# Performance work log

Hardware: AMD Instinct MI355X
Metric: run time of the kernel (lower is better)

## Reference

```python
import jax, jax.numpy as jnp
import numpy as np

N = 100000
E = 600000
D_IN, D_HID, D_OUT = 128, 128, 64


def setup_inputs() -> dict:
    key = jax.random.key(0)
    k1, k2, k3, k4 = jax.random.split(key, 4)
    x = jax.random.normal(k1, (N, D_IN), dtype=jnp.float32)
    edge_index = jax.random.randint(k2, (2, E), 0, N, dtype=jnp.int64)
    edge_weight = jnp.ones((E,), dtype=jnp.float32)
    W1 = jax.random.normal(k3, (D_IN, D_HID), dtype=jnp.float32) / np.sqrt(D_IN)
    b1 = jnp.zeros((D_HID,), dtype=jnp.float32)
    W2 = jax.random.normal(k4, (D_HID, D_OUT), dtype=jnp.float32) / np.sqrt(D_HID)
    b2 = jnp.zeros((D_OUT,), dtype=jnp.float32)
    return {"x": x, "edge_index": edge_index, "edge_weight": edge_weight,
            "W1": W1, "b1": b1, "W2": W2, "b2": b2}


def _gcn_conv(x, row, col, ew, W, b, n_nodes):
    # x: [N, d_in]; row/col/ew include self loops. PyG gcn_norm:
    # deg[i] = sum of ew over edges with target i; norm = d^-1/2[row]*ew*d^-1/2[col]
    deg = jax.ops.segment_sum(ew, col, num_segments=n_nodes)
    dinv = jnp.where(deg > 0, jax.lax.rsqrt(deg), 0.0)
    norm = dinv[row] * ew * dinv[col]  # [E+N]
    xw = x @ W  # dense transform first (d_out <= d_in path)
    msg = xw[row] * norm[:, None]  # gather + scale  [E+N, d_out]
    out = jax.ops.segment_sum(msg, col, num_segments=n_nodes)  # scatter-add
    return out + b


def reference(x, edge_index, edge_weight, W1, b1, W2, b2):
    n = x.shape[0]
    loops = jnp.arange(n, dtype=edge_index.dtype)
    row = jnp.concatenate([edge_index[0], loops])
    col = jnp.concatenate([edge_index[1], loops])
    ew = jnp.concatenate([edge_weight, jnp.ones((n,), dtype=edge_weight.dtype)])
    # dropout is identity in eval mode
    h = jax.nn.relu(_gcn_conv(x, row, col, ew, W1, b1, n))
    out = _gcn_conv(h, row, col, ew, W2, b2, n)
    return out
```

## Files before the change

### kernel.cpp

```cpp
#include <hip/hip_runtime.h>


constexpr int SCAN_BLOCKS = 256;

typedef __attribute__((ext_vector_type(8))) short short8;
typedef __attribute__((ext_vector_type(4))) float f32x4;

__device__ __forceinline__ ushort f2bf(float f) {
    unsigned u = __float_as_uint(f);
    return (ushort)((u + 0x7fffu + ((u >> 16) & 1u)) >> 16);
}
__device__ __forceinline__ float bf2f(ushort h) {
    return __uint_as_float((unsigned)h << 16);
}

__global__ __launch_bounds__(256) void prep_kernel(
        int* __restrict__ cnt, int N,
        const float* __restrict__ W2, ushort* __restrict__ W2t) {
    const int n4 = (N >> 2) + 1;
    const int nbz = (n4 + 255) / 256;
    int b = blockIdx.x;
    if (b < nbz) {
        const int i = b * 256 + threadIdx.x;
        if (i < n4) reinterpret_cast<int4*>(cnt)[i] = make_int4(0, 0, 0, 0);
        return;
    }
    b -= nbz;
    const int o = b * 256 + threadIdx.x;
    if (o < 64 * 128)
        W2t[o] = f2bf(W2[(size_t)(o & 127) * 64 + (o >> 7)]);
}

__global__ __launch_bounds__(256, 2) void combo_kernel(
        const float* __restrict__ X, const float* __restrict__ W1,
        ushort* __restrict__ Ab, int N, int G,
        const int* __restrict__ col, int* __restrict__ cnt,
        int* __restrict__ rank, int E) {
    __shared__ __align__(16) ushort sX[128 * 128];
    __shared__ __align__(16) ushort sW[128 * 128];
    const int tid = threadIdx.x;

    if (blockIdx.x >= G) {
        const int e4 = ((blockIdx.x - G) * 256 + tid) * 4;
        if (e4 + 3 < E) {
            const int4 c4 = *reinterpret_cast<const int4*>(col + e4);
            int4 r4;
            r4.x = atomicAdd(&cnt[c4.x], 1);
            r4.y = atomicAdd(&cnt[c4.y], 1);
            r4.z = atomicAdd(&cnt[c4.z], 1);
            r4.w = atomicAdd(&cnt[c4.w], 1);
            *reinterpret_cast<int4*>(rank + e4) = r4;
        } else {
            for (int e = e4; e < E; e++) rank[e] = atomicAdd(&cnt[col[e]], 1);
        }
        return;
    }

    const int base = blockIdx.x * 128;
    #pragma unroll
    for (int p = 0; p < 8; p++) {
        const int ch = p * 256 + tid;
        const int r = ch >> 4, cpos = ch & 15;
        const int grow = base + r;
        uint4 u = make_uint4(0, 0, 0, 0);
        if (grow < N) {
            const float* xp = X + (size_t)grow * 128 + cpos * 8;
            const float4 a = *reinterpret_cast<const float4*>(xp);
            const float4 c = *reinterpret_cast<const float4*>(xp + 4);
            u.x = (uint)f2bf(a.x) | ((uint)f2bf(a.y) << 16);
            u.y = (uint)f2bf(a.z) | ((uint)f2bf(a.w) << 16);
            u.z = (uint)f2bf(c.x) | ((uint)f2bf(c.y) << 16);
            u.w = (uint)f2bf(c.z) | ((uint)f2bf(c.w) << 16);
        }
        const int b = (cpos * 16) ^ ((r & 7) << 4);
        *reinterpret_cast<uint4*>(reinterpret_cast<char*>(sX) + r * 256 + b) = u;
    }
    #pragma unroll
    for (int p = 0; p < 8; p++) {
        const int ch = p * 256 + tid;
        const int c = ch & 127, kc = ch >> 7;
        const int k0 = kc * 8;
        float f[8];
        #pragma unroll
        for (int j = 0; j < 8; j++) f[j] = W1[(size_t)(k0 + j) * 128 + c];
        uint4 u;
        u.x = (uint)f2bf(f[0]) | ((uint)f2bf(f[1]) << 16);
        u.y = (uint)f2bf(f[2]) | ((uint)f2bf(f[3]) << 16);
        u.z = (uint)f2bf(f[4]) | ((uint)f2bf(f[5]) << 16);
        u.w = (uint)f2bf(f[6]) | ((uint)f2bf(f[7]) << 16);
        const int b = (k0 * 2) ^ ((c & 7) << 4);
        *reinterpret_cast<uint4*>(reinterpret_cast<char*>(sW) + c * 256 + b) = u;
    }
    __syncthreads();

    const int lane = tid & 63;
    const int wid = tid >> 6;
    const int wr = wid >> 1;
    const int wc = wid & 1;
    const int lr = lane & 15;
    const int g  = lane >> 4;

    f32x4 acc[4][4];
    #pragma unroll
    for (int i = 0; i < 4; i++)
        #pragma unroll
        for (int f = 0; f < 4; f++) acc[i][f] = (f32x4){0.f, 0.f, 0.f, 0.f};

    #pragma unroll
    for (int ks = 0; ks < 4; ks++) {
        const int koff = ks * 64 + g * 16;
        short8 a[4], b[4];
        #pragma unroll
        for (int i = 0; i < 4; i++) {
            const int r = wr * 64 + i * 16 + lr;
            a[i] = *reinterpret_cast<const short8*>(
                reinterpret_cast<const char*>(sX) + r * 256 + (koff ^ ((r & 7) << 4)));
        }
        #pragma unroll
        for (int f = 0; f < 4; f++) {
            const int c = wc * 64 + f * 16 + lr;
            b[f] = *reinterpret_cast<const short8*>(
                reinterpret_cast<const char*>(sW) + c * 256 + (koff ^ ((c & 7) << 4)));
        }
        #pragma unroll
        for (int i = 0; i < 4; i++)
            #pragma unroll
            for (int f = 0; f < 4; f++)
                acc[i][f] = __builtin_amdgcn_mfma_f32_16x16x32_bf16(a[i], b[f], acc[i][f], 0, 0, 0);
    }

    #pragma unroll
    for (int i = 0; i < 4; i++)
        #pragma unroll
        for (int reg = 0; reg < 4; reg++) {
            const int grow = base + wr * 64 + i * 16 + g * 4 + reg;
            if (grow < N)
                #pragma unroll
                for (int f = 0; f < 4; f++)
                    Ab[(size_t)grow * 128 + wc * 64 + f * 16 + lr] = f2bf(acc[i][f][reg]);
        }
}

__global__ __launch_bounds__(256) void scan_kernel(
        const int* __restrict__ cnt, int* __restrict__ rowptr,
        int* __restrict__ partial, int* __restrict__ flag, int N, int E) {
    const int t = threadIdx.x, b = blockIdx.x;
    const int T = SCAN_BLOCKS * 256;
    const int chunk = (N + T - 1) / T;
    const int j = b * 256 + t;
    const int s = min(j * chunk, N), e = min(s + chunk, N);
    int acc = 0;
    for (int i = s; i < e; i++) acc += cnt[i];

    __shared__ int sh[256];
    sh[t] = acc;
    __syncthreads();
    for (int off = 1; off < 256; off <<= 1) {
        int x = sh[t];
        int a = (t >= off) ? sh[t - off] : 0;
        __syncthreads();
        sh[t] = x + a;
        __syncthreads();
    }
    const int thr_excl = sh[t] - acc;
    if (t == 255) partial[b] = sh[255];
    __syncthreads();
    if (t == 0) {
        __threadfence();
        atomicAdd(flag, 1);
        while (__hip_atomic_load(flag, __ATOMIC_RELAXED,
                                 __HIP_MEMORY_SCOPE_AGENT) < SCAN_BLOCKS) {}
    }
    __syncthreads();

    __shared__ int tp[256];
    tp[t] = __hip_atomic_load(&partial[t], __ATOMIC_RELAXED,
                              __HIP_MEMORY_SCOPE_AGENT);
    __syncthreads();
    for (int off = 1; off < 256; off <<= 1) {
        int x = tp[t];
        int a = (t >= off) ? tp[t - off] : 0;
        __syncthreads();
        tp[t] = x + a;
        __syncthreads();
    }
    int run = ((b == 0) ? 0 : tp[b - 1]) + thr_excl;
    for (int i = s; i < e; i++) { rowptr[i] = run; run += cnt[i]; }
    if (j == 0) rowptr[N] = E;
}

__global__ void fill_kernel(const int* __restrict__ row, const int* __restrict__ col,
        const float* __restrict__ ew, const int* __restrict__ rowptr,
        const int* __restrict__ rank, int2* __restrict__ csr, int E) {
    const int e4 = (blockIdx.x * blockDim.x + threadIdx.x) * 4;
    if (e4 + 3 < E) {
        const int4 c4 = *reinterpret_cast<const int4*>(col + e4);
        const int4 r4 = *reinterpret_cast<const int4*>(row + e4);
        const int4 w4 = *reinterpret_cast<const int4*>((const int*)ew + e4);
        const int4 k4 = *reinterpret_cast<const int4*>(rank + e4);
        const int p0 = rowptr[c4.x] + k4.x;
        const int p1 = rowptr[c4.y] + k4.y;
        const int p2 = rowptr[c4.z] + k4.z;
        const int p3 = rowptr[c4.w] + k4.w;
        csr[p0] = make_int2(r4.x, w4.x);
        csr[p1] = make_int2(r4.y, w4.y);
        csr[p2] = make_int2(r4.z, w4.z);
        csr[p3] = make_int2(r4.w, w4.w);
    } else {
        for (int e = e4; e < E; e++)
            csr[rowptr[col[e]] + rank[e]] = make_int2(row[e], __float_as_int(ew[e]));
    }
}

__global__ __launch_bounds__(256) void degsum_kernel(
        const int* __restrict__ rowptr, const int2* __restrict__ csr,
        float* __restrict__ dinv, int N) {
    const int n = blockIdx.x * blockDim.x + threadIdx.x;
    if (n >= N) return;
    const int e0 = rowptr[n], e1 = rowptr[n + 1];
    float d = 1.0f;
    for (int e = e0; e < e1; e++) d += __int_as_float(csr[e].y);
    dinv[n] = (d > 0.0f) ? rsqrtf(d) : 0.0f;
}

__global__ __launch_bounds__(256) void agg1_kernel(
        const int* __restrict__ rowptr, const int2* __restrict__ csr,
        const float* __restrict__ dinv,
        const ushort* __restrict__ src, const float* __restrict__ bias,
        ushort* __restrict__ dst, int N) {
    const int gid = blockIdx.x * 256 + threadIdx.x;
    const int c = gid >> 4;
    if (c >= N) return;
    const int lane = gid & 15;
    const float di = dinv[c];
    const float sl = di * di;
    float acc[8];
    {
        const short8 s8 = *reinterpret_cast<const short8*>(src + (size_t)c * 128 + lane * 8);
        #pragma unroll
        for (int j = 0; j < 8; j++) acc[j] = bf2f((ushort)s8[j]) * sl;
    }
    const int e0 = rowptr[c], e1 = rowptr[c + 1];
    int e = e0;
    for (; e + 4 <= e1; e += 4) {
        const int2 c0 = csr[e], c1 = csr[e + 1], c2 = csr[e + 2], c3 = csr[e + 3];
        const float w0 = __int_as_float(c0.y) * dinv[c0.x] * di;
        const float w1 = __int_as_float(c1.y) * dinv[c1.x] * di;
        const float w2 = __int_as_float(c2.y) * dinv[c2.x] * di;
        const float w3 = __int_as_float(c3.y) * dinv[c3.x] * di;
        const short8 v0 = *reinterpret_cast<const short8*>(src + (size_t)c0.x * 128 + lane * 8);
        const short8 v1 = *reinterpret_cast<const short8*>(src + (size_t)c1.x * 128 + lane * 8);
        const short8 v2 = *reinterpret_cast<const short8*>(src + (size_t)c2.x * 128 + lane * 8);
        const short8 v3 = *reinterpret_cast<const short8*>(src + (size_t)c3.x * 128 + lane * 8);
        #pragma unroll
        for (int j = 0; j < 8; j++)
            acc[j] += bf2f((ushort)v0[j]) * w0 + bf2f((ushort)v1[j]) * w1 +
                      bf2f((ushort)v2[j]) * w2 + bf2f((ushort)v3[j]) * w3;
    }
    for (; e < e1; e++) {
        const int2 ce = csr[e];
        const float w = __int_as_float(ce.y) * dinv[ce.x] * di;
        const short8 v = *reinterpret_cast<const short8*>(src + (size_t)ce.x * 128 + lane * 8);
        #pragma unroll
        for (int j = 0; j < 8; j++) acc[j] += bf2f((ushort)v[j]) * w;
    }
    const float4 b0 = reinterpret_cast<const float4*>(bias)[lane * 2];
    const float4 b1 = reinterpret_cast<const float4*>(bias)[lane * 2 + 1];
    acc[0] = fmaxf(acc[0] + b0.x, 0.f); acc[1] = fmaxf(acc[1] + b0.y, 0.f);
    acc[2] = fmaxf(acc[2] + b0.z, 0.f); acc[3] = fmaxf(acc[3] + b0.w, 0.f);
    acc[4] = fmaxf(acc[4] + b1.x, 0.f); acc[5] = fmaxf(acc[5] + b1.y, 0.f);
    acc[6] = fmaxf(acc[6] + b1.z, 0.f); acc[7] = fmaxf(acc[7] + b1.w, 0.f);
    uint4 o;
    o.x = (uint)f2bf(acc[0]) | ((uint)f2bf(acc[1]) << 16);
    o.y = (uint)f2bf(acc[2]) | ((uint)f2bf(acc[3]) << 16);
    o.z = (uint)f2bf(acc[4]) | ((uint)f2bf(acc[5]) << 16);
    o.w = (uint)f2bf(acc[6]) | ((uint)f2bf(acc[7]) << 16);
    *reinterpret_cast<uint4*>(dst + (size_t)c * 128 + lane * 8) = o;
}

__global__ __launch_bounds__(256, 2) void gemm2_kernel(
        const ushort* __restrict__ Xb, const ushort* __restrict__ Wt,
        ushort* __restrict__ Y, int N) {
    __shared__ __align__(16) ushort sX[128 * 128];
    __shared__ __align__(16) ushort sW[64 * 128];
    const int tid = threadIdx.x;
    const int base = blockIdx.x * 128;

    #pragma unroll
    for (int p = 0; p < 8; p++) {
        const int ch = p * 256 + tid;
        const int r = ch >> 4, cpos = ch & 15;
        const int grow = base + r;
        uint4 v = make_uint4(0, 0, 0, 0);
        if (grow < N)
            v = *reinterpret_cast<const uint4*>(Xb + (size_t)grow * 128 + cpos * 8);
        const int b = (cpos * 16) ^ ((r & 7) << 4);
        *reinterpret_cast<uint4*>(reinterpret_cast<char*>(sX) + r * 256 + b) = v;
    }
    #pragma unroll
    for (int p = 0; p < 4; p++) {
        const int ch = p * 256 + tid;
        const int r = ch >> 4, cpos = ch & 15;
        uint4 v = *reinterpret_cast<const uint4*>(Wt + (size_t)r * 128 + cpos * 8);
        const int b = (cpos * 16) ^ ((r & 7) << 4);
        *reinterpret_cast<uint4*>(reinterpret_cast<char*>(sW) + r * 256 + b) = v;
    }
    __syncthreads();

    const int lane = tid & 63;
    const int wid = tid >> 6;
    const int lr = lane & 15;
    const int g  = lane >> 4;

    f32x4 acc[2][4];
    #pragma unroll
    for (int i = 0; i < 2; i++)
        #pragma unroll
        for (int f = 0; f < 4; f++) acc[i][f] = (f32x4){0.f, 0.f, 0.f, 0.f};

    #pragma unroll
    for (int ks = 0; ks < 4; ks++) {
        const int koff = ks * 64 + g * 16;
        short8 a[2], b[4];
        #pragma unroll
        for (int i = 0; i < 2; i++) {
            const int r = wid * 32 + i * 16 + lr;
            a[i] = *reinterpret_cast<const short8*>(
                reinterpret_cast<const char*>(sX) + r * 256 + (koff ^ ((r & 7) << 4)));
        }
        #pragma unroll
        for (int f = 0; f < 4; f++) {
            const int c = f * 16 + lr;
            b[f] = *reinterpret_cast<const short8*>(
                reinterpret_cast<const char*>(sW) + c * 256 + (koff ^ ((c & 7) << 4)));
        }
        #pragma unroll
        for (int i = 0; i < 2; i++)
            #pragma unroll
            for (int f = 0; f < 4; f++)
                acc[i][f] = __builtin_amdgcn_mfma_f32_16x16x32_bf16(a[i], b[f], acc[i][f], 0, 0, 0);
    }

    #pragma unroll
    for (int i = 0; i < 2; i++)
        #pragma unroll
        for (int reg = 0; reg < 4; reg++) {
            const int grow = base + wid * 32 + i * 16 + g * 4 + reg;
            if (grow < N)
                #pragma unroll
                for (int f = 0; f < 4; f++)
                    Y[(size_t)grow * 64 + f * 16 + lr] = f2bf(acc[i][f][reg]);
        }
}

__global__ __launch_bounds__(256) void agg2_kernel(
        const int* __restrict__ rowptr, const int2* __restrict__ csr,
        const float* __restrict__ dinv,
        const ushort* __restrict__ src, const float* __restrict__ bias,
        float* __restrict__ dst, int N) {
    const int gid = blockIdx.x * 256 + threadIdx.x;
    const int c = gid >> 3;
    if (c >= N) return;
    const int lane = gid & 7;
    const float di = dinv[c];
    const float sl = di * di;
    float acc[8];
    {
        const short8 s8 = *reinterpret_cast<const short8*>(src + (size_t)c * 64 + lane * 8);
        #pragma unroll
        for (int j = 0; j < 8; j++) acc[j] = bf2f((ushort)s8[j]) * sl;
    }
    const int e0 = rowptr[c], e1 = rowptr[c + 1];
    int e = e0;
    for (; e + 4 <= e1; e += 4) {
        const int2 c0 = csr[e], c1 = csr[e + 1], c2 = csr[e + 2], c3 = csr[e + 3];
        const float w0 = __int_as_float(c0.y) * dinv[c0.x] * di;
        const float w1 = __int_as_float(c1.y) * dinv[c1.x] * di;
        const float w2 = __int_as_float(c2.y) * dinv[c2.x] * di;
        const float w3 = __int_as_float(c3.y) * dinv[c3.x] * di;
        const short8 v0 = *reinterpret_cast<const short8*>(src + (size_t)c0.x * 64 + lane * 8);
        const short8 v1 = *reinterpret_cast<const short8*>(src + (size_t)c1.x * 64 + lane * 8);
        const short8 v2 = *reinterpret_cast<const short8*>(src + (size_t)c2.x * 64 + lane * 8);
        const short8 v3 = *reinterpret_cast<const short8*>(src + (size_t)c3.x * 64 + lane * 8);
        #pragma unroll
        for (int j = 0; j < 8; j++)
            acc[j] += bf2f((ushort)v0[j]) * w0 + bf2f((ushort)v1[j]) * w1 +
                      bf2f((ushort)v2[j]) * w2 + bf2f((ushort)v3[j]) * w3;
    }
    for (; e < e1; e++) {
        const int2 ce = csr[e];
        const float w = __int_as_float(ce.y) * dinv[ce.x] * di;
        const short8 v = *reinterpret_cast<const short8*>(src + (size_t)ce.x * 64 + lane * 8);
        #pragma unroll
        for (int j = 0; j < 8; j++) acc[j] += bf2f((ushort)v[j]) * w;
    }
    const float4 b0 = reinterpret_cast<const float4*>(bias)[lane * 2];
    const float4 b1 = reinterpret_cast<const float4*>(bias)[lane * 2 + 1];
    float* dp = dst + (size_t)c * 64 + lane * 8;
    *reinterpret_cast<float4*>(dp) =
        make_float4(acc[0] + b0.x, acc[1] + b0.y, acc[2] + b0.z, acc[3] + b0.w);
    *reinterpret_cast<float4*>(dp + 4) =
        make_float4(acc[4] + b1.x, acc[5] + b1.y, acc[6] + b1.z, acc[7] + b1.w);
}

extern "C" void kernel_launch(void* const* d_in, const int* in_sizes, int n_in,
                              void* d_out, int out_size, void* d_ws, size_t ws_size,
                              hipStream_t stream) {
    const float* x  = (const float*)d_in[0];
    const int*   ei = (const int*)d_in[1];
    const float* ew = (const float*)d_in[2];
    const float* W1 = (const float*)d_in[3];
    const float* b1 = (const float*)d_in[4];
    const float* W2 = (const float*)d_in[5];
    const float* b2 = (const float*)d_in[6];
    const int N = in_sizes[0] / 128;
    const int E = in_sizes[1] / 2;
    const int* row = ei;
    const int* col = ei + E;

    char* w = (char*)d_ws;
    float* dinv = (float*)w;                 w += (size_t)N * 4;
    ushort* Ab  = (ushort*)w;                w += (size_t)N * 256;
    ushort* Hb  = (ushort*)w;                w += (size_t)N * 256;
    ushort* Gb  = (ushort*)w;                w += (size_t)N * 128;
    ushort* W2t = (ushort*)w;                w += 64 * 128 * 2;
    int* cnt    = (int*)w;                   w += (size_t)N * 4 + 16;
    int* rowptr = (int*)w;                   w += (size_t)(N + 8) * 4;
    int* partial= (int*)w;                   w += 2048 * 4;
    int* rank   = (int*)w;                   w += (size_t)E * 4;
    int2* csr   = (int2*)w;
    float* out  = (float*)d_out;
    int* flag   = cnt + N;

    const int ntiles = (N + 127) / 128;
    const int nbz = ((N >> 2) + 1 + 255) / 256;
    const int eb4 = (E / 4 + 255) / 256;

    prep_kernel<<<nbz + 32, 256, 0, stream>>>(cnt, N, W2, W2t);
    combo_kernel<<<ntiles + eb4, 256, 0, stream>>>(x, W1, Ab, N, ntiles,
                                                   col, cnt, rank, E);
    scan_kernel<<<SCAN_BLOCKS, 256, 0, stream>>>(cnt, rowptr, partial, flag, N, E);
    fill_kernel<<<eb4, 256, 0, stream>>>(row, col, ew, rowptr, rank, csr, E);
    degsum_kernel<<<(N + 255) / 256, 256, 0, stream>>>(rowptr, csr, dinv, N);
    agg1_kernel<<<(N * 16 + 255) / 256, 256, 0, stream>>>(rowptr, csr, dinv, Ab, b1, Hb, N);
    gemm2_kernel<<<ntiles, 256, 0, stream>>>(Hb, W2t, Gb, N);
    agg2_kernel<<<(N * 8 + 255) / 256, 256, 0, stream>>>(rowptr, csr, dinv, Gb, b2, out, N);
}
```

Before: 142.7 us.

## Fuse scan, CSR fill and degree into one kernel with grid barriers

Moves the cnt zeroing and W2 transpose into the GEMM1 launch and splits edge counting into its own kernel. Scan, CSR fill and degree computation now run in a single persistent 256-block kernel separated by software grid barriers. The aim is to cut launch overhead and inter-kernel gaps. In exchange, fill and degree work runs on only 256 blocks with grid-stride loops, which may lower parallelism, and the counting atomics no longer overlap with the GEMM.

```diff
diff --git a/kernel.cpp b/kernel.cpp
--- a/kernel.cpp
+++ b/kernel.cpp
@@ -14,44 +14,38 @@
     return __uint_as_float((unsigned)h << 16);
 }
 
-__global__ __launch_bounds__(256) void prep_kernel(
-        int* __restrict__ cnt, int N,
-        const float* __restrict__ W2, ushort* __restrict__ W2t) {
-    const int n4 = (N >> 2) + 1;
-    const int nbz = (n4 + 255) / 256;
-    int b = blockIdx.x;
-    if (b < nbz) {
-        const int i = b * 256 + threadIdx.x;
-        if (i < n4) reinterpret_cast<int4*>(cnt)[i] = make_int4(0, 0, 0, 0);
-        return;
-    }
-    b -= nbz;
-    const int o = b * 256 + threadIdx.x;
-    if (o < 64 * 128)
-        W2t[o] = f2bf(W2[(size_t)(o & 127) * 64 + (o >> 7)]);
-}
-
-__global__ __launch_bounds__(256, 2) void combo_kernel(
+__device__ __forceinline__ void grid_bar(int* flag, int target) {
+    __syncthreads();
+    if (threadIdx.x == 0) {
+        __threadfence();
+        atomicAdd(flag, 1);
+        while (__hip_atomic_load(flag, __ATOMIC_RELAXED,
+                                 __HIP_MEMORY_SCOPE_AGENT) < target) {}
+    }
+    __syncthreads();
+    __threadfence();
+}
+
+__global__ __launch_bounds__(256, 2) void gemm1_kernel(
         const float* __restrict__ X, const float* __restrict__ W1,
         ushort* __restrict__ Ab, int N, int G,
-        const int* __restrict__ col, int* __restrict__ cnt,
-        int* __restrict__ rank, int E) {
+        int* __restrict__ cnt, const float* __restrict__ W2,
+        ushort* __restrict__ W2t) {
     __shared__ __align__(16) ushort sX[128 * 128];
     __shared__ __align__(16) ushort sW[128 * 128];
     const int tid = threadIdx.x;
 
     if (blockIdx.x >= G) {
-        const int e4 = ((blockIdx.x - G) * 256 + tid) * 4;
-        if (e4 + 3 < E) {
-            const int4 c4 = *reinterpret_cast<const int4*>(col + e4);
-            int4 r4;
-            r4.x = atomicAdd(&cnt[c4.x], 1);
-            r4.y = atomicAdd(&cnt[c4.y], 1);
-            r4.z = atomicAdd(&cnt[c4.z], 1);
-            r4.w = atomicAdd(&cnt[c4.w], 1);
-            *reinterpret_cast<int4*>(rank + e4) = r4;
+        const int b = blockIdx.x - G;
+        const int n4 = (N >> 2) + 1;
+        const int nbz = (n4 + 255) / 256;
+        if (b < nbz) {
+            const int i = b * 256 + tid;
+            if (i < n4) reinterpret_cast<int4*>(cnt)[i] = make_int4(0, 0, 0, 0);
         } else {
-            for (int e = e4; e < E; e++) rank[e] = atomicAdd(&cnt[col[e]], 1);
+            const int o = (b - nbz) * 256 + tid;
+            if (o < 64 * 128)
+                W2t[o] = f2bf(W2[(size_t)(o & 127) * 64 + (o >> 7)]);
         }
         return;
     }
@@ -141,17 +135,36 @@
         }
 }
 
-__global__ __launch_bounds__(256) void scan_kernel(
+__global__ void cnt_kernel(const int* __restrict__ col, int* __restrict__ cnt,
+                           int* __restrict__ rank, int E) {
+    const int e4 = (blockIdx.x * blockDim.x + threadIdx.x) * 4;
+    if (e4 + 3 < E) {
+        const int4 c4 = *reinterpret_cast<const int4*>(col + e4);
+        int4 r4;
+        r4.x = atomicAdd(&cnt[c4.x], 1);
+        r4.y = atomicAdd(&cnt[c4.y], 1);
+        r4.z = atomicAdd(&cnt[c4.z], 1);
+        r4.w = atomicAdd(&cnt[c4.w], 1);
+        *reinterpret_cast<int4*>(rank + e4) = r4;
+    } else {
+        for (int e = e4; e < E; e++) rank[e] = atomicAdd(&cnt[col[e]], 1);
+    }
+}
+
+__global__ __launch_bounds__(256) void sfd_kernel(
         const int* __restrict__ cnt, int* __restrict__ rowptr,
-        int* __restrict__ partial, int* __restrict__ flag, int N, int E) {
+        int* __restrict__ partial, int* __restrict__ flags,
+        const int* __restrict__ row, const int* __restrict__ col,
+        const float* __restrict__ ew, const int* __restrict__ rank,
+        int2* __restrict__ csr, float* __restrict__ dinv, int N, int E) {
     const int t = threadIdx.x, b = blockIdx.x;
     const int T = SCAN_BLOCKS * 256;
+    const int gtid = b * 256 + t;
     const int chunk = (N + T - 1) / T;
-    const int j = b * 256 + t;
-    const int s = min(j * chunk, N), e = min(s + chunk, N);
+    const int s = min(gtid * chunk, N), e = min(s + chunk, N);
+
     int acc = 0;
     for (int i = s; i < e; i++) acc += cnt[i];
-
     __shared__ int sh[256];
     sh[t] = acc;
     __syncthreads();
@@ -164,18 +177,10 @@
     }
     const int thr_excl = sh[t] - acc;
     if (t == 255) partial[b] = sh[255];
-    __syncthreads();
-    if (t == 0) {
-        __threadfence();
-        atomicAdd(flag, 1);
-        while (__hip_atomic_load(flag, __ATOMIC_RELAXED,
-                                 __HIP_MEMORY_SCOPE_AGENT) < SCAN_BLOCKS) {}
-    }
-    __syncthreads();
+    grid_bar(&flags[0], SCAN_BLOCKS);
 
     __shared__ int tp[256];
-    tp[t] = __hip_atomic_load(&partial[t], __ATOMIC_RELAXED,
-                              __HIP_MEMORY_SCOPE_AGENT);
+    tp[t] = partial[t];
     __syncthreads();
     for (int off = 1; off < 256; off <<= 1) {
         int x = tp[t];
@@ -186,41 +191,39 @@
     }
     int run = ((b == 0) ? 0 : tp[b - 1]) + thr_excl;
     for (int i = s; i < e; i++) { rowptr[i] = run; run += cnt[i]; }
-    if (j == 0) rowptr[N] = E;
-}
-
-__global__ void fill_kernel(const int* __restrict__ row, const int* __restrict__ col,
-        const float* __restrict__ ew, const int* __restrict__ rowptr,
-        const int* __restrict__ rank, int2* __restrict__ csr, int E) {
-    const int e4 = (blockIdx.x * blockDim.x + threadIdx.x) * 4;
-    if (e4 + 3 < E) {
-        const int4 c4 = *reinterpret_cast<const int4*>(col + e4);
-        const int4 r4 = *reinterpret_cast<const int4*>(row + e4);
-        const int4 w4 = *reinterpret_cast<const int4*>((const int*)ew + e4);
-        const int4 k4 = *reinterpret_cast<const int4*>(rank + e4);
-        const int p0 = rowptr[c4.x] + k4.x;
-        const int p1 = rowptr[c4.y] + k4.y;
-        const int p2 = rowptr[c4.z] + k4.z;
-        const int p3 = rowptr[c4.w] + k4.w;
-        csr[p0] = make_int2(r4.x, w4.x);
-        csr[p1] = make_int2(r4.y, w4.y);
-        csr[p2] = make_int2(r4.z, w4.z);
-        csr[p3] = make_int2(r4.w, w4.w);
-    } else {
-        for (int e = e4; e < E; e++)
-            csr[rowptr[col[e]] + rank[e]] = make_int2(row[e], __float_as_int(ew[e]));
-    }
-}
-
-__global__ __launch_bounds__(256) void degsum_kernel(
-        const int* __restrict__ rowptr, const int2* __restrict__ csr,
-        float* __restrict__ dinv, int N) {
-    const int n = blockIdx.x * blockDim.x + threadIdx.x;
-    if (n >= N) return;
-    const int e0 = rowptr[n], e1 = rowptr[n + 1];
-    float d = 1.0f;
-    for (int e = e0; e < e1; e++) d += __int_as_float(csr[e].y);
-    dinv[n] = (d > 0.0f) ? rsqrtf(d) : 0.0f;
+    if (gtid == 0) rowptr[N] = E;
+    grid_bar(&flags[1], SCAN_BLOCKS);
+
+    const int ngrp = (E + 3) >> 2;
+    for (int g = gtid; g < ngrp; g += T) {
+        const int e4 = g * 4;
+        if (e4 + 3 < E) {
+            const int4 c4 = *reinterpret_cast<const int4*>(col + e4);
+            const int4 r4 = *reinterpret_cast<const int4*>(row + e4);
+            const int4 w4 = *reinterpret_cast<const int4*>((const int*)ew + e4);
+            const int4 k4 = *reinterpret_cast<const int4*>(rank + e4);
+            const int p0 = rowptr[c4.x] + k4.x;
+            const int p1 = rowptr[c4.y] + k4.y;
+            const int p2 = rowptr[c4.z] + k4.z;
+            const int p3 = rowptr[c4.w] + k4.w;
+            csr[p0] = make_int2(r4.x, w4.x);
+            csr[p1] = make_int2(r4.y, w4.y);
+            csr[p2] = make_int2(r4.z, w4.z);
+            csr[p3] = make_int2(r4.w, w4.w);
+        } else {
+            for (int ee = e4; ee < E; ee++)
+                csr[rowptr[col[ee]] + rank[ee]] =
+                    make_int2(row[ee], __float_as_int(ew[ee]));
+        }
+    }
+    grid_bar(&flags[2], SCAN_BLOCKS);
+
+    for (int n = gtid; n < N; n += T) {
+        const int e0 = rowptr[n], e1 = rowptr[n + 1];
+        float d = 1.0f;
+        for (int k = e0; k < e1; k++) d += __int_as_float(csr[k].y);
+        dinv[n] = (d > 0.0f) ? rsqrtf(d) : 0.0f;
+    }
 }
 
 __global__ __launch_bounds__(256) void agg1_kernel(
@@ -430,18 +433,17 @@
     int* rank   = (int*)w;                   w += (size_t)E * 4;
     int2* csr   = (int2*)w;
     float* out  = (float*)d_out;
-    int* flag   = cnt + N;
+    int* flags  = cnt + N;
 
     const int ntiles = (N + 127) / 128;
     const int nbz = ((N >> 2) + 1 + 255) / 256;
     const int eb4 = (E / 4 + 255) / 256;
 
-    prep_kernel<<<nbz + 32, 256, 0, stream>>>(cnt, N, W2, W2t);
-    combo_kernel<<<ntiles + eb4, 256, 0, stream>>>(x, W1, Ab, N, ntiles,
-                                                   col, cnt, rank, E);
-    scan_kernel<<<SCAN_BLOCKS, 256, 0, stream>>>(cnt, rowptr, partial, flag, N, E);
-    fill_kernel<<<eb4, 256, 0, stream>>>(row, col, ew, rowptr, rank, csr, E);
-    degsum_kernel<<<(N + 255) / 256, 256, 0, stream>>>(rowptr, csr, dinv, N);
+    gemm1_kernel<<<ntiles + nbz + 32, 256, 0, stream>>>(x, W1, Ab, N, ntiles,
+                                                        cnt, W2, W2t);
+    cnt_kernel<<<eb4, 256, 0, stream>>>(col, cnt, rank, E);
+    sfd_kernel<<<SCAN_BLOCKS, 256, 0, stream>>>(cnt, rowptr, partial, flags,
+                                                row, col, ew, rank, csr, dinv, N, E);
     agg1_kernel<<<(N * 16 + 255) / 256, 256, 0, stream>>>(rowptr, csr, dinv, Ab, b1, Hb, N);
     gemm2_kernel<<<ntiles, 256, 0, stream>>>(Hb, W2t, Gb, N);
     agg2_kernel<<<(N * 8 + 255) / 256, 256, 0, stream>>>(rowptr, csr, dinv, Gb, b2, out, N);
```

Measured after the change: 226.5 us. 1.59x slower.
